# Optimization experiments

Measured on AMD Instinct MI355X. Metric: run time of the kernel, lower is better.

## Reference

```python
import jax, jax.numpy as jnp
import numpy as np

N_USERS = 70000
N_ITEMS = 30000
N = N_USERS + N_ITEMS
E = 1280000
EMB = 64
N_LAYERS = 3
EPS = 0.1


def setup_inputs() -> dict:
    key = jax.random.key(0)
    k1, k2, k3, k4 = jax.random.split(key, 4)
    ego_embeddings = jax.random.normal(k1, (N, EMB), dtype=jnp.float32) * 0.1
    edge_row = jax.random.randint(k2, (E,), 0, N, dtype=jnp.int32)
    edge_col = jax.random.randint(k3, (E,), 0, N, dtype=jnp.int32)
    # normalized-adjacency-like positive weights
    edge_val = jax.random.uniform(k4, (E,), dtype=jnp.float32) * 0.1
    return {"ego_embeddings": ego_embeddings, "edge_row": edge_row,
            "edge_col": edge_col, "edge_val": edge_val}


def _spmm(edge_row, edge_col, edge_val, x):
    # out[r] = sum_{e: row[e]=r} val[e] * x[col[e]]
    gathered = edge_val[:, None] * x[edge_col]          # [E, EMB]
    return jax.ops.segment_sum(gathered, edge_row, num_segments=N)


def _l2_normalize(x, axis=-1):
    # matches F.normalize: x / max(||x||, 1e-12)
    norm = jnp.sqrt(jnp.sum(x * x, axis=axis, keepdims=True))
    return x / jnp.maximum(norm, 1e-12)


def reference(ego_embeddings, edge_row, edge_col, edge_val):
    noise_key = jax.random.key(42)
    acc = jnp.zeros_like(ego_embeddings)
    ego = ego_embeddings
    for k in range(N_LAYERS):
        ego = _spmm(edge_row, edge_col, edge_val, ego)
        # perturbed=True branch: torch.rand_like -> uniform [0,1)
        noise = jax.random.uniform(jax.random.fold_in(noise_key, k),
                                   ego.shape, dtype=ego.dtype)
        ego = ego + jnp.sign(ego) * _l2_normalize(noise) * EPS
        acc = acc + ego
    all_embeddings = acc / N_LAYERS  # mean over stacked layers
    user_all_embeddings = all_embeddings[:N_USERS]
    item_all_embeddings = all_embeddings[N_USERS:]
    return (user_all_embeddings, item_all_embeddings)
```

## Files before the change

kernel.cpp:

```cpp
#include <hip/hip_runtime.h>
#include <stdint.h>

static constexpr int NT    = 100000;
static constexpr int EMB_D = 64;
static constexpr float EPS_F = 0.1f;

__host__ __device__ inline uint32_t rotl32(uint32_t v, int d) {
  return (v << d) | (v >> (32 - d));
}

__host__ __device__ inline void tf2x32(uint32_t k0, uint32_t k1,
                                       uint32_t c0, uint32_t c1,
                                       uint32_t& o0, uint32_t& o1) {
  uint32_t ks0 = k0, ks1 = k1, ks2 = k0 ^ k1 ^ 0x1BD11BDAu;
  uint32_t x0 = c0 + ks0, x1 = c1 + ks1;
  const int ra[4] = {13, 15, 26, 6};
  const int rb[4] = {17, 29, 16, 24};
#pragma unroll
  for (int i = 0; i < 4; i++) { x0 += x1; x1 = rotl32(x1, ra[i]); x1 ^= x0; }
  x0 += ks1; x1 += ks2 + 1u;
#pragma unroll
  for (int i = 0; i < 4; i++) { x0 += x1; x1 = rotl32(x1, rb[i]); x1 ^= x0; }
  x0 += ks2; x1 += ks0 + 2u;
#pragma unroll
  for (int i = 0; i < 4; i++) { x0 += x1; x1 = rotl32(x1, ra[i]); x1 ^= x0; }
  x0 += ks0; x1 += ks1 + 3u;
#pragma unroll
  for (int i = 0; i < 4; i++) { x0 += x1; x1 = rotl32(x1, rb[i]); x1 ^= x0; }
  x0 += ks1; x1 += ks2 + 4u;
#pragma unroll
  for (int i = 0; i < 4; i++) { x0 += x1; x1 = rotl32(x1, ra[i]); x1 ^= x0; }
  x0 += ks2; x1 += ks0 + 5u;
  o0 = x0; o1 = x1;
}

__device__ inline float tf_uniform(uint32_t fk0, uint32_t fk1, uint32_t idx) {
  uint32_t o0, o1;
  tf2x32(fk0, fk1, 0u, idx, o0, o1);
  uint32_t bits = o0 ^ o1;
  return __uint_as_float((bits >> 9) | 0x3F800000u) - 1.0f;
}

__global__ __launch_bounds__(256) void rank_kernel(
    const int* __restrict__ erow, int* __restrict__ cnt,
    int* __restrict__ rank, int nE) {
  const int base = blockIdx.x * 2048 + threadIdx.x;
  int r[8], rk[8];
#pragma unroll
  for (int i = 0; i < 8; i++) {
    const int e = base + i * 256;
    r[i] = (e < nE) ? erow[e] : -1;
  }
#pragma unroll
  for (int i = 0; i < 8; i++)
    if (r[i] >= 0) rk[i] = atomicAdd(&cnt[r[i]], 1);
#pragma unroll
  for (int i = 0; i < 8; i++) {
    const int e = base + i * 256;
    if (e < nE) rank[e] = rk[i];
  }
}

static constexpr int SCAN_CHUNK = 2048;
static constexpr int SCAN_T     = 256;
static constexpr int SCAN_NB    = (NT + SCAN_CHUNK - 1) / SCAN_CHUNK;

__global__ __launch_bounds__(SCAN_T) void scan_reduce(
    const int* __restrict__ cnt, int* __restrict__ partial) {
  __shared__ int lds[SCAN_T];
  int base = blockIdx.x * SCAN_CHUNK + threadIdx.x * 8;
  int s = 0;
#pragma unroll
  for (int i = 0; i < 8; i++) { int idx = base + i; if (idx < NT) s += cnt[idx]; }
  lds[threadIdx.x] = s; __syncthreads();
  for (int off = SCAN_T / 2; off > 0; off >>= 1) {
    if (threadIdx.x < off) lds[threadIdx.x] += lds[threadIdx.x + off];
    __syncthreads();
  }
  if (threadIdx.x == 0) partial[blockIdx.x] = lds[0];
}

__global__ __launch_bounds__(64) void scan_offsets(
    const int* __restrict__ partial, int* __restrict__ offsets, int nb) {
  if (threadIdx.x == 0) {
    int run = 0;
    for (int b = 0; b < nb; b++) { offsets[b] = run; run += partial[b]; }
    offsets[nb] = run;
  }
}

__global__ __launch_bounds__(SCAN_T) void scan_write(
    const int* __restrict__ cnt, const int* __restrict__ offsets,
    int* __restrict__ row_ptr) {
  __shared__ int lds[SCAN_T];
  const int tid  = threadIdx.x;
  const int base = blockIdx.x * SCAN_CHUNK + tid * 8;
  int v[8]; int s = 0;
#pragma unroll
  for (int i = 0; i < 8; i++) { int idx = base + i; v[i] = (idx < NT) ? cnt[idx] : 0; s += v[i]; }
  lds[tid] = s; __syncthreads();
  for (int off = 1; off < SCAN_T; off <<= 1) {
    int t = 0;
    if (tid >= off) t = lds[tid - off];
    __syncthreads();
    if (tid >= off) lds[tid] += t;
    __syncthreads();
  }
  const int excl = lds[tid] - s;
  int run = offsets[blockIdx.x] + excl;
#pragma unroll
  for (int i = 0; i < 8; i++) {
    int idx = base + i;
    if (idx < NT) { row_ptr[idx] = run; run += v[i]; }
  }
  if (blockIdx.x == gridDim.x - 1 && tid == SCAN_T - 1)
    row_ptr[NT] = offsets[gridDim.x];
}

__global__ __launch_bounds__(256) void scatter2_kernel(
    const int* __restrict__ erow, const int* __restrict__ ecol,
    const float* __restrict__ eval_, const int* __restrict__ rank,
    const int* __restrict__ rptr, int2* __restrict__ pk, int nE) {
  const int base = blockIdx.x * 2048 + threadIdx.x;
#pragma unroll
  for (int i = 0; i < 8; i++) {
    const int e = base + i * 256;
    if (e < nE) {
      const int r = erow[e];
      const int p = rptr[r] + rank[e];
      int2 w; w.x = ecol[e]; w.y = __float_as_int(eval_[e]);
      pk[p] = w;
    }
  }
}

__global__ __launch_bounds__(256) void spmm_noise_kernel(
    const int* __restrict__ row_ptr, const int2* __restrict__ pk,
    const float* __restrict__ x,
    float* __restrict__ ego_out, float* __restrict__ acc,
    uint32_t fk0, uint32_t fk1, int mode) {
  const int row = blockIdx.x * 8 + (threadIdx.x >> 5);
  if (row >= NT) return;
  const int l32 = threadIdx.x & 31;

  const int beg = row_ptr[row];
  const int end = row_ptr[row + 1];

  float s0 = 0.0f, s1 = 0.0f;
  int j = beg;
  for (; j + 8 <= end; j += 8) {
    int2 p[8]; float2 xv[8];
#pragma unroll
    for (int i = 0; i < 8; i++) p[i] = pk[j + i];
#pragma unroll
    for (int i = 0; i < 8; i++)
      xv[i] = *reinterpret_cast<const float2*>(&x[(size_t)p[i].x * EMB_D + 2 * l32]);
#pragma unroll
    for (int i = 0; i < 8; i++) {
      const float v = __int_as_float(p[i].y);
      s0 = fmaf(v, xv[i].x, s0); s1 = fmaf(v, xv[i].y, s1);
    }
  }
  for (; j + 2 <= end; j += 2) {
    const int2 p0 = pk[j], p1 = pk[j + 1];
    const float2 x0 = *reinterpret_cast<const float2*>(&x[(size_t)p0.x * EMB_D + 2 * l32]);
    const float2 x1 = *reinterpret_cast<const float2*>(&x[(size_t)p1.x * EMB_D + 2 * l32]);
    const float v0 = __int_as_float(p0.y), v1 = __int_as_float(p1.y);
    s0 = fmaf(v0, x0.x, s0); s1 = fmaf(v0, x0.y, s1);
    s0 = fmaf(v1, x1.x, s0); s1 = fmaf(v1, x1.y, s1);
  }
  if (j < end) {
    const int2 p = pk[j];
    const float2 xv = *reinterpret_cast<const float2*>(&x[(size_t)p.x * EMB_D + 2 * l32]);
    const float v = __int_as_float(p.y);
    s0 = fmaf(v, xv.x, s0); s1 = fmaf(v, xv.y, s1);
  }

  const uint32_t idx = (uint32_t)row * EMB_D + 2 * l32;
  const float u0 = tf_uniform(fk0, fk1, idx);
  const float u1 = tf_uniform(fk0, fk1, idx + 1);
  float nsq = u0 * u0 + u1 * u1;
#pragma unroll
  for (int m = 1; m < 32; m <<= 1) nsq += __shfl_xor(nsq, m);
  const float rinv = 1.0f / fmaxf(sqrtf(nsq), 1e-12f);

  const float sg0 = (s0 > 0.0f) ? 1.0f : ((s0 < 0.0f) ? -1.0f : 0.0f);
  const float sg1 = (s1 > 0.0f) ? 1.0f : ((s1 < 0.0f) ? -1.0f : 0.0f);
  float2 en;
  en.x = s0 + sg0 * (u0 * rinv) * EPS_F;
  en.y = s1 + sg1 * (u1 * rinv) * EPS_F;

  float2* accp = reinterpret_cast<float2*>(&acc[idx]);
  if (mode == 0) {
    *reinterpret_cast<float2*>(&ego_out[idx]) = en;
    *accp = en;
  } else if (mode == 1) {
    *reinterpret_cast<float2*>(&ego_out[idx]) = en;
    float2 a = *accp; a.x += en.x; a.y += en.y; *accp = a;
  } else {
    float2 a = *accp;
    a.x = (a.x + en.x) * (1.0f / 3.0f);
    a.y = (a.y + en.y) * (1.0f / 3.0f);
    *accp = a;
  }
}

__global__ __launch_bounds__(256) void spmm_kernel(
    const int* __restrict__ erow, const int* __restrict__ ecol,
    const float* __restrict__ eval_, const float* __restrict__ x,
    float* __restrict__ y, int nE) {
  const int lane = threadIdx.x & 63;
  const int wave = (blockIdx.x * blockDim.x + threadIdx.x) >> 6;
  const int nWav = (gridDim.x * blockDim.x) >> 6;
  for (int e = wave; e < nE; e += nWav) {
    const int r = erow[e];
    const int c = ecol[e];
    const float v = eval_[e];
    unsafeAtomicAdd(&y[r * EMB_D + lane], v * x[c * EMB_D + lane]);
  }
}

__global__ __launch_bounds__(256) void noise_acc_kernel(
    float* __restrict__ ego, float* __restrict__ acc,
    uint32_t fk0, uint32_t fk1, int mode) {
  const int row = blockIdx.x * 4 + (threadIdx.x >> 6);
  if (row >= NT) return;
  const int lane = threadIdx.x & 63;
  const int idx  = row * EMB_D + lane;
  const float u = tf_uniform(fk0, fk1, (uint32_t)idx);
  float nsq = u * u;
#pragma unroll
  for (int m = 1; m < 64; m <<= 1) nsq += __shfl_xor(nsq, m, 64);
  const float un = u / fmaxf(sqrtf(nsq), 1e-12f);
  const float e  = ego[idx];
  const float sg = (e > 0.0f) ? 1.0f : ((e < 0.0f) ? -1.0f : 0.0f);
  const float en = e + sg * un * EPS_F;
  ego[idx] = en;
  if (mode == 0)      acc[idx] = en;
  else if (mode == 1) acc[idx] = acc[idx] + en;
  else                acc[idx] = (acc[idx] + en) * (1.0f / 3.0f);
}

extern "C" void kernel_launch(void* const* d_in, const int* in_sizes, int n_in,
                              void* d_out, int out_size, void* d_ws, size_t ws_size,
                              hipStream_t stream) {
  const float* ego_in = (const float*)d_in[0];
  const int*   erow   = (const int*)d_in[1];
  const int*   ecol   = (const int*)d_in[2];
  const float* eval_  = (const float*)d_in[3];
  const int nE = in_sizes[1];

  float* out = (float*)d_out;

  uint32_t fk[3][2];
  for (uint32_t k = 0; k < 3; k++) tf2x32(0u, 42u, 0u, k, fk[k][0], fk[k][1]);

  const size_t egoElems = (size_t)NT * EMB_D;

  float* bufA = (float*)d_ws;
  float* bufB = bufA + egoElems;
  int2*  pk   = (int2*)(bufB + egoElems);
  int*   rptr = (int*)(pk + nE);
  int*   cnt  = rptr + (NT + 1);
  int*   part = cnt + NT;
  int*   offs = part + 64;
  const size_t needBytes = (char*)(offs + 64) - (char*)d_ws;

  int* rank = (int*)bufA;

  if (ws_size >= needBytes) {
    hipMemsetAsync(cnt, 0, (size_t)NT * sizeof(int), stream);
    const int eb8 = (nE + 2047) / 2048;
    rank_kernel<<<eb8, 256, 0, stream>>>(erow, cnt, rank, nE);
    scan_reduce<<<SCAN_NB, SCAN_T, 0, stream>>>(cnt, part);
    scan_offsets<<<1, 64, 0, stream>>>(part, offs, SCAN_NB);
    scan_write<<<SCAN_NB, SCAN_T, 0, stream>>>(cnt, offs, rptr);
    scatter2_kernel<<<eb8, 256, 0, stream>>>(erow, ecol, eval_, rank, rptr, pk, nE);

    const int nb = (NT + 7) / 8;
    spmm_noise_kernel<<<nb, 256, 0, stream>>>(rptr, pk, ego_in, bufA, out,
                                              fk[0][0], fk[0][1], 0);
    spmm_noise_kernel<<<nb, 256, 0, stream>>>(rptr, pk, bufA, bufB, out,
                                              fk[1][0], fk[1][1], 1);
    spmm_noise_kernel<<<nb, 256, 0, stream>>>(rptr, pk, bufB, nullptr, out,
                                              fk[2][0], fk[2][1], 2);
  } else {
    const size_t bytes = egoElems * sizeof(float);
    const int noiseBlocks = (NT + 3) / 4;
    hipMemsetAsync(bufA, 0, bytes, stream);
    spmm_kernel<<<2048, 256, 0, stream>>>(erow, ecol, eval_, ego_in, bufA, nE);
    noise_acc_kernel<<<noiseBlocks, 256, 0, stream>>>(bufA, out, fk[0][0], fk[0][1], 0);
    hipMemsetAsync(bufB, 0, bytes, stream);
    spmm_kernel<<<2048, 256, 0, stream>>>(erow, ecol, eval_, bufA, bufB, nE);
    noise_acc_kernel<<<noiseBlocks, 256, 0, stream>>>(bufB, out, fk[1][0], fk[1][1], 1);
    hipMemsetAsync(bufA, 0, bytes, stream);
    spmm_kernel<<<2048, 256, 0, stream>>>(erow, ecol, eval_, bufB, bufA, nE);
    noise_acc_kernel<<<noiseBlocks, 256, 0, stream>>>(bufA, out, fk[2][0], fk[2][1], 2);
  }
}
```

Before: 338.4 us.

## Drop accumulator round-trips, use float4 half-wave rows, and fuse scan offsets

Layers one and two no longer read and write the accumulator; they only write their ego output. The final layer reads both earlier layer buffers and writes the averaged result directly. The SpMM now assigns 16 lanes per row with float4 gathers instead of 32 lanes with float2. The separate single-thread offsets kernel is removed, and each scan_write block reduces the preceding partials itself with a wave shuffle. This cuts global memory traffic and one launch, at the cost of more Threefry work per lane.

```diff
diff --git a/kernel.cpp b/kernel.cpp
--- a/kernel.cpp
+++ b/kernel.cpp
@@ -47,6 +47,8 @@
   const int base = blockIdx.x * 2048 + threadIdx.x;
   int r[8], rk[8];
 #pragma unroll
+  for (int i = 0; i < 8; i++) rk[i] = 0;
+#pragma unroll
   for (int i = 0; i < 8; i++) {
     const int e = base + i * 256;
     r[i] = (e < nE) ? erow[e] : -1;
@@ -80,20 +82,18 @@
   if (threadIdx.x == 0) partial[blockIdx.x] = lds[0];
 }
 
-__global__ __launch_bounds__(64) void scan_offsets(
-    const int* __restrict__ partial, int* __restrict__ offsets, int nb) {
-  if (threadIdx.x == 0) {
-    int run = 0;
-    for (int b = 0; b < nb; b++) { offsets[b] = run; run += partial[b]; }
-    offsets[nb] = run;
-  }
-}
-
 __global__ __launch_bounds__(SCAN_T) void scan_write(
-    const int* __restrict__ cnt, const int* __restrict__ offsets,
+    const int* __restrict__ cnt, const int* __restrict__ partial,
     int* __restrict__ row_ptr) {
   __shared__ int lds[SCAN_T];
-  const int tid  = threadIdx.x;
+  __shared__ int base_sh;
+  const int tid = threadIdx.x;
+  if (tid < 64) {
+    int pv = (tid < blockIdx.x) ? partial[tid] : 0;
+#pragma unroll
+    for (int m = 1; m < 64; m <<= 1) pv += __shfl_xor(pv, m, 64);
+    if (tid == 0) base_sh = pv;
+  }
   const int base = blockIdx.x * SCAN_CHUNK + tid * 8;
   int v[8]; int s = 0;
 #pragma unroll
@@ -107,14 +107,14 @@
     __syncthreads();
   }
   const int excl = lds[tid] - s;
-  int run = offsets[blockIdx.x] + excl;
+  int run = base_sh + excl;
 #pragma unroll
   for (int i = 0; i < 8; i++) {
     int idx = base + i;
     if (idx < NT) { row_ptr[idx] = run; run += v[i]; }
   }
   if (blockIdx.x == gridDim.x - 1 && tid == SCAN_T - 1)
-    row_ptr[NT] = offsets[gridDim.x];
+    row_ptr[NT] = base_sh + lds[SCAN_T - 1];
 }
 
 __global__ __launch_bounds__(256) void scatter2_kernel(
@@ -137,72 +137,84 @@
 __global__ __launch_bounds__(256) void spmm_noise_kernel(
     const int* __restrict__ row_ptr, const int2* __restrict__ pk,
     const float* __restrict__ x,
-    float* __restrict__ ego_out, float* __restrict__ acc,
-    uint32_t fk0, uint32_t fk1, int mode) {
-  const int row = blockIdx.x * 8 + (threadIdx.x >> 5);
+    const float* __restrict__ aA, const float* __restrict__ aB,
+    float* __restrict__ outp,
+    uint32_t fk0, uint32_t fk1) {
+  const int row = blockIdx.x * 16 + (threadIdx.x >> 4);
   if (row >= NT) return;
-  const int l32 = threadIdx.x & 31;
+  const int l16 = threadIdx.x & 15;
 
   const int beg = row_ptr[row];
   const int end = row_ptr[row + 1];
 
-  float s0 = 0.0f, s1 = 0.0f;
+  float s0 = 0.0f, s1 = 0.0f, s2 = 0.0f, s3 = 0.0f;
   int j = beg;
   for (; j + 8 <= end; j += 8) {
-    int2 p[8]; float2 xv[8];
+    int2 p[8];
 #pragma unroll
     for (int i = 0; i < 8; i++) p[i] = pk[j + i];
+    float4 xv[8];
 #pragma unroll
     for (int i = 0; i < 8; i++)
-      xv[i] = *reinterpret_cast<const float2*>(&x[(size_t)p[i].x * EMB_D + 2 * l32]);
+      xv[i] = *reinterpret_cast<const float4*>(
+          &x[((size_t)(uint32_t)p[i].x << 6) + 4 * l16]);
 #pragma unroll
     for (int i = 0; i < 8; i++) {
       const float v = __int_as_float(p[i].y);
       s0 = fmaf(v, xv[i].x, s0); s1 = fmaf(v, xv[i].y, s1);
+      s2 = fmaf(v, xv[i].z, s2); s3 = fmaf(v, xv[i].w, s3);
     }
   }
   for (; j + 2 <= end; j += 2) {
     const int2 p0 = pk[j], p1 = pk[j + 1];
-    const float2 x0 = *reinterpret_cast<const float2*>(&x[(size_t)p0.x * EMB_D + 2 * l32]);
-    const float2 x1 = *reinterpret_cast<const float2*>(&x[(size_t)p1.x * EMB_D + 2 * l32]);
+    const float4 x0 = *reinterpret_cast<const float4*>(
+        &x[((size_t)(uint32_t)p0.x << 6) + 4 * l16]);
+    const float4 x1 = *reinterpret_cast<const float4*>(
+        &x[((size_t)(uint32_t)p1.x << 6) + 4 * l16]);
     const float v0 = __int_as_float(p0.y), v1 = __int_as_float(p1.y);
     s0 = fmaf(v0, x0.x, s0); s1 = fmaf(v0, x0.y, s1);
+    s2 = fmaf(v0, x0.z, s2); s3 = fmaf(v0, x0.w, s3);
     s0 = fmaf(v1, x1.x, s0); s1 = fmaf(v1, x1.y, s1);
+    s2 = fmaf(v1, x1.z, s2); s3 = fmaf(v1, x1.w, s3);
   }
   if (j < end) {
     const int2 p = pk[j];
-    const float2 xv = *reinterpret_cast<const float2*>(&x[(size_t)p.x * EMB_D + 2 * l32]);
+    const float4 xv = *reinterpret_cast<const float4*>(
+        &x[((size_t)(uint32_t)p.x << 6) + 4 * l16]);
     const float v = __int_as_float(p.y);
     s0 = fmaf(v, xv.x, s0); s1 = fmaf(v, xv.y, s1);
-  }
-
-  const uint32_t idx = (uint32_t)row * EMB_D + 2 * l32;
+    s2 = fmaf(v, xv.z, s2); s3 = fmaf(v, xv.w, s3);
+  }
+
+  const uint32_t idx = (uint32_t)row * EMB_D + 4 * l16;
   const float u0 = tf_uniform(fk0, fk1, idx);
   const float u1 = tf_uniform(fk0, fk1, idx + 1);
-  float nsq = u0 * u0 + u1 * u1;
-#pragma unroll
-  for (int m = 1; m < 32; m <<= 1) nsq += __shfl_xor(nsq, m);
+  const float u2 = tf_uniform(fk0, fk1, idx + 2);
+  const float u3 = tf_uniform(fk0, fk1, idx + 3);
+  float nsq = u0 * u0 + u1 * u1 + u2 * u2 + u3 * u3;
+#pragma unroll
+  for (int m = 1; m < 16; m <<= 1) nsq += __shfl_xor(nsq, m);
   const float rinv = 1.0f / fmaxf(sqrtf(nsq), 1e-12f);
 
   const float sg0 = (s0 > 0.0f) ? 1.0f : ((s0 < 0.0f) ? -1.0f : 0.0f);
   const float sg1 = (s1 > 0.0f) ? 1.0f : ((s1 < 0.0f) ? -1.0f : 0.0f);
-  float2 en;
+  const float sg2 = (s2 > 0.0f) ? 1.0f : ((s2 < 0.0f) ? -1.0f : 0.0f);
+  const float sg3 = (s3 > 0.0f) ? 1.0f : ((s3 < 0.0f) ? -1.0f : 0.0f);
+  float4 en;
   en.x = s0 + sg0 * (u0 * rinv) * EPS_F;
   en.y = s1 + sg1 * (u1 * rinv) * EPS_F;
-
-  float2* accp = reinterpret_cast<float2*>(&acc[idx]);
-  if (mode == 0) {
-    *reinterpret_cast<float2*>(&ego_out[idx]) = en;
-    *accp = en;
-  } else if (mode == 1) {
-    *reinterpret_cast<float2*>(&ego_out[idx]) = en;
-    float2 a = *accp; a.x += en.x; a.y += en.y; *accp = a;
-  } else {
-    float2 a = *accp;
-    a.x = (a.x + en.x) * (1.0f / 3.0f);
-    a.y = (a.y + en.y) * (1.0f / 3.0f);
-    *accp = a;
-  }
+  en.z = s2 + sg2 * (u2 * rinv) * EPS_F;
+  en.w = s3 + sg3 * (u3 * rinv) * EPS_F;
+
+  if (aA != nullptr) {
+    const float4 a = *reinterpret_cast<const float4*>(&aA[idx]);
+    const float4 b = *reinterpret_cast<const float4*>(&aB[idx]);
+    en.x = ((a.x + b.x) + en.x) * (1.0f / 3.0f);
+    en.y = ((a.y + b.y) + en.y) * (1.0f / 3.0f);
+    en.z = ((a.z + b.z) + en.z) * (1.0f / 3.0f);
+    en.w = ((a.w + b.w) + en.w) * (1.0f / 3.0f);
+  }
+  *reinterpret_cast<float4*>(&outp[idx]) = en;
 }
 
 __global__ __launch_bounds__(256) void spmm_kernel(
@@ -263,8 +275,7 @@
   int*   rptr = (int*)(pk + nE);
   int*   cnt  = rptr + (NT + 1);
   int*   part = cnt + NT;
-  int*   offs = part + 64;
-  const size_t needBytes = (char*)(offs + 64) - (char*)d_ws;
+  const size_t needBytes = (char*)(part + 64) - (char*)d_ws;
 
   int* rank = (int*)bufA;
 
@@ -273,17 +284,16 @@
     const int eb8 = (nE + 2047) / 2048;
     rank_kernel<<<eb8, 256, 0, stream>>>(erow, cnt, rank, nE);
     scan_reduce<<<SCAN_NB, SCAN_T, 0, stream>>>(cnt, part);
-    scan_offsets<<<1, 64, 0, stream>>>(part, offs, SCAN_NB);
-    scan_write<<<SCAN_NB, SCAN_T, 0, stream>>>(cnt, offs, rptr);
+    scan_write<<<SCAN_NB, SCAN_T, 0, stream>>>(cnt, part, rptr);
     scatter2_kernel<<<eb8, 256, 0, stream>>>(erow, ecol, eval_, rank, rptr, pk, nE);
 
-    const int nb = (NT + 7) / 8;
-    spmm_noise_kernel<<<nb, 256, 0, stream>>>(rptr, pk, ego_in, bufA, out,
-                                              fk[0][0], fk[0][1], 0);
-    spmm_noise_kernel<<<nb, 256, 0, stream>>>(rptr, pk, bufA, bufB, out,
-                                              fk[1][0], fk[1][1], 1);
-    spmm_noise_kernel<<<nb, 256, 0, stream>>>(rptr, pk, bufB, nullptr, out,
-                                              fk[2][0], fk[2][1], 2);
+    const int nb = (NT + 15) / 16;
+    spmm_noise_kernel<<<nb, 256, 0, stream>>>(rptr, pk, ego_in, nullptr, nullptr,
+                                              bufA, fk[0][0], fk[0][1]);
+    spmm_noise_kernel<<<nb, 256, 0, stream>>>(rptr, pk, bufA, nullptr, nullptr,
+                                              bufB, fk[1][0], fk[1][1]);
+    spmm_noise_kernel<<<nb, 256, 0, stream>>>(rptr, pk, bufB, bufA, bufB,
+                                              out, fk[2][0], fk[2][1]);
   } else {
     const size_t bytes = egoElems * sizeof(float);
     const int noiseBlocks = (NT + 3) / 4;
```

Measured after the change: 321.3 us. 1.05x faster.
